# Performance work log

Hardware: AMD Instinct MI355X
Metric: run time of the kernel (lower is better)

Reference implementation:

```python
import jax, jax.numpy as jnp
import numpy as np

B, N, C_IN = 4, 2048, 256
H, C_HEAD = 8, 32  # c_out=256, concat=True -> 256//8=32 per head
ALPHA = 0.2
NEG_INF = -9e15

def glorot(key, shape, fan_in, fan_out):
    lim = jnp.sqrt(6.0 / (fan_in + fan_out))
    return jax.random.uniform(key, shape, jnp.float32, -lim, lim)

def setup_inputs() -> dict:
    key = jax.random.key(0)
    k1, k2, k3, k4, k5 = jax.random.split(key, 5)
    x = jax.random.normal(k1, (B, N, C_IN), jnp.float32)
    G = jax.random.randint(k2, (B, N, N), 0, 2, jnp.int32)
    # ensure self-loops so no row is fully masked
    eye = jnp.eye(N, dtype=jnp.int32)[None]
    G = jnp.maximum(G, eye)
    proj_kernel = glorot(k3, (C_IN, H * C_HEAD), C_IN, H * C_HEAD)
    proj_bias = jnp.zeros((H * C_HEAD,), jnp.float32)
    attn_fst = glorot(k4, (H, C_HEAD), H, C_HEAD)
    attn_snd = glorot(k5, (H, C_HEAD), H, C_HEAD)
    return {"x": x, "G": G, "proj_kernel": proj_kernel, "proj_bias": proj_bias,
            "attn_fst": attn_fst, "attn_snd": attn_snd}

def reference(x, G, proj_kernel, proj_bias, attn_fst, attn_snd):
    b, n = x.shape[0], x.shape[1]
    h = (x @ proj_kernel + proj_bias).reshape(b, n, H, C_HEAD)  # [B,N,H,c]
    lf = jnp.einsum('bnhc,hc->bnh', h, attn_fst)  # [B,N,H]
    ls = jnp.einsum('bnhc,hc->bnh', h, attn_snd)  # [B,N,H]
    logit = lf[:, :, None, :] + ls[:, None, :, :]  # [B,N,N,H]
    logit = jax.nn.leaky_relu(logit, negative_slope=ALPHA)
    logit = jnp.where(G[..., None] == 1, logit, NEG_INF)
    attn = jax.nn.softmax(logit, axis=2)
    out = jnp.einsum('bijh,bjhc->bihc', attn, h)  # [B,N,H,c]
    return out.reshape(b, n, H * C_HEAD)  # concat=True
```

## Files before the change

kernel.cpp:

```cpp
#include <hip/hip_runtime.h>

#define BB 4
#define NN 2048
#define CIN 256
#define HH 8
#define COUT 256
#define ALPHAc 0.2f
#define TI 8
#define CJ 64

#define PBM 128
#define PBN 64
#define PKT 16
#define XLD (PBM + 4)
__global__ __launch_bounds__(256) void gat_proj(
    const float* __restrict__ x, const float* __restrict__ W,
    const float* __restrict__ bias, const float* __restrict__ afst,
    const float* __restrict__ asnd, float* __restrict__ hout,
    float* __restrict__ lfout, float* __restrict__ lsout)
{
    __shared__ float xsT[PKT][XLD];
    __shared__ float wls[PKT][PBN];
    const int t = threadIdx.x;
    const int bx = blockIdx.x & 3;
    const int by = blockIdx.x >> 2;
    const int row0 = by * PBM, col0 = bx * PBN;
    const int tx = t & 15, ty = t >> 4;

    float acc[8][4];
#pragma unroll
    for (int i = 0; i < 8; ++i)
#pragma unroll
        for (int j = 0; j < 4; ++j) acc[i][j] = 0.f;

    for (int kt = 0; kt < CIN; kt += PKT) {
#pragma unroll
        for (int s = 0; s < 2; ++s) {
            const int idx = s * 256 + t;
            const int row = idx >> 2, kq = (idx & 3) * 4;
            const float4 v = *(const float4*)(x + (size_t)(row0 + row) * CIN + kt + kq);
            xsT[kq + 0][row] = v.x; xsT[kq + 1][row] = v.y;
            xsT[kq + 2][row] = v.z; xsT[kq + 3][row] = v.w;
        }
        {
            const int k = t >> 4, c4 = (t & 15) * 4;
            *(float4*)&wls[k][c4] = *(const float4*)(W + (size_t)(kt + k) * COUT + col0 + c4);
        }
        __syncthreads();
#pragma unroll
        for (int k = 0; k < PKT; ++k) {
            float xv[8], wv[4];
            *(float4*)&xv[0] = *(const float4*)&xsT[k][ty * 8];
            *(float4*)&xv[4] = *(const float4*)&xsT[k][ty * 8 + 4];
            *(float4*)&wv[0] = *(const float4*)&wls[k][tx * 4];
#pragma unroll
            for (int i = 0; i < 8; ++i)
#pragma unroll
                for (int j = 0; j < 4; ++j)
                    acc[i][j] = fmaf(xv[i], wv[j], acc[i][j]);
        }
        __syncthreads();
    }

    const float4 bv = *(const float4*)(bias + col0 + tx * 4);
    const float4 af = *(const float4*)(afst + col0 + tx * 4);
    const float4 as = *(const float4*)(asnd + col0 + tx * 4);
    const int hd = (col0 + tx * 4) >> 5;
#pragma unroll
    for (int i = 0; i < 8; ++i) {
        float4 o;
        o.x = acc[i][0] + bv.x; o.y = acc[i][1] + bv.y;
        o.z = acc[i][2] + bv.z; o.w = acc[i][3] + bv.w;
        const int row = row0 + ty * 8 + i;
        *(float4*)(hout + (size_t)row * COUT + col0 + tx * 4) = o;
        float pf = o.x * af.x + o.y * af.y + o.z * af.z + o.w * af.w;
        float ps = o.x * as.x + o.y * as.y + o.z * as.z + o.w * as.w;
#pragma unroll
        for (int off = 1; off < 8; off <<= 1) {
            pf += __shfl_xor(pf, off);
            ps += __shfl_xor(ps, off);
        }
        if ((tx & 7) == 0) {
            lfout[(size_t)row * HH + hd] = pf;
            lsout[(size_t)row * HH + hd] = ps;
        }
    }
}

__device__ __forceinline__ int eoff4(int jl, int h, int half) {
    return jl * 64 + ((((h << 1) + half) ^ (jl & 7)) << 2);
}

__global__ __launch_bounds__(256) void gat_attn(
    const int* __restrict__ G, const float* __restrict__ hin,
    const float* __restrict__ lf, const float* __restrict__ ls,
    float* __restrict__ out)
{
    __shared__ __align__(16) float e_lds[CJ * 64];
    __shared__ unsigned g_lds[4][CJ];
    __shared__ float lf_lds[TI][HH];
    __shared__ float s_lds[TI][HH];

    const int t = threadIdx.x;
    const int b = blockIdx.x / (NN / TI);
    const int i0 = (blockIdx.x % (NN / TI)) * TI;
    const int h = t >> 5;
    const int jj = t & 31;
    const int w = t >> 6;
    const int l = t & 63;
    const int hh = l >> 3;

    if (t < TI * HH)
        lf_lds[t >> 3][t & 7] = lf[(size_t)(b * NN + i0 + (t >> 3)) * HH + (t & 7)];

    float sp[TI];
    float a[TI][4];
#pragma unroll
    for (int r = 0; r < TI; ++r) {
        sp[r] = 0.f;
#pragma unroll
        for (int c2 = 0; c2 < 4; ++c2) a[r][c2] = 0.f;
    }
    __syncthreads();
    float lfv[TI];
#pragma unroll
    for (int r = 0; r < TI; ++r) lfv[r] = lf_lds[r][h];

    for (int j0 = 0; j0 < NN; j0 += CJ) {
        {
            const int col = t & 63;
            const int* gp = G + (size_t)(b * NN + i0 + 2 * w) * NN + j0 + col;
            g_lds[w][col] = (gp[0] != 0 ? 1u : 0u) | (gp[NN] != 0 ? 2u : 0u);
        }
        __syncthreads();
#pragma unroll
        for (int k = 0; k < CJ / 32; ++k) {
            const int jl = jj + 32 * k;
            const float lsv = ls[(size_t)(b * NN + j0 + jl) * HH + h];
            const unsigned gm = g_lds[0][jl] | (g_lds[1][jl] << 2) |
                                (g_lds[2][jl] << 4) | (g_lds[3][jl] << 6);
            float ev[TI];
#pragma unroll
            for (int r = 0; r < TI; ++r) {
                float xv = lfv[r] + lsv;
                xv = xv > 0.f ? xv : ALPHAc * xv;
                ev[r] = ((gm >> r) & 1u) ? __expf(xv) : 0.f;
                sp[r] += ev[r];
            }
            *(float4*)&e_lds[eoff4(jl, h, 0)] = make_float4(ev[0], ev[1], ev[2], ev[3]);
            *(float4*)&e_lds[eoff4(jl, h, 1)] = make_float4(ev[4], ev[5], ev[6], ev[7]);
        }
        __syncthreads();
        {
            const float* hbase = hin + (size_t)(b * NN + j0) * COUT + (l << 2);
            float4 hnext = *(const float4*)(hbase + (size_t)w * COUT);
#pragma unroll
            for (int it = 0; it < CJ / 4; ++it) {
                const int jl = w + it * 4;
                const float4 hv = hnext;
                if (it + 1 < CJ / 4)
                    hnext = *(const float4*)(hbase + (size_t)(jl + 4) * COUT);
                const float4 lo = *(const float4*)&e_lds[eoff4(jl, hh, 0)];
                const float4 hi = *(const float4*)&e_lds[eoff4(jl, hh, 1)];
                const float ee[8] = {lo.x, lo.y, lo.z, lo.w, hi.x, hi.y, hi.z, hi.w};
                const float hvv[4] = {hv.x, hv.y, hv.z, hv.w};
#pragma unroll
                for (int r = 0; r < TI; ++r)
#pragma unroll
                    for (int c2 = 0; c2 < 4; ++c2)
                        a[r][c2] = fmaf(ee[r], hvv[c2], a[r][c2]);
            }
        }
        __syncthreads();
    }
#pragma unroll
    for (int off = 16; off; off >>= 1) {
#pragma unroll
        for (int r = 0; r < TI; ++r) sp[r] += __shfl_xor(sp[r], off);
    }
    if (jj == 0) {
#pragma unroll
        for (int r = 0; r < TI; ++r) s_lds[r][h] = sp[r];
    }
    float* buf = e_lds;
    if (w >= 2) {
#pragma unroll
        for (int r = 0; r < TI; ++r)
#pragma unroll
            for (int c2 = 0; c2 < 4; ++c2)
                buf[((w - 2) << 11) + ((r * 4 + c2) << 6) + l] = a[r][c2];
    }
    __syncthreads();
    if (w < 2) {
#pragma unroll
        for (int r = 0; r < TI; ++r)
#pragma unroll
            for (int c2 = 0; c2 < 4; ++c2)
                a[r][c2] += buf[(w << 11) + ((r * 4 + c2) << 6) + l];
    }
    __syncthreads();
    if (w == 1) {
#pragma unroll
        for (int r = 0; r < TI; ++r)
#pragma unroll
            for (int c2 = 0; c2 < 4; ++c2)
                buf[((r * 4 + c2) << 6) + l] = a[r][c2];
    }
    __syncthreads();
    if (w == 0) {
#pragma unroll
        for (int r = 0; r < TI; ++r) {
            const float inv = 1.f / s_lds[r][hh];
            float4 o;
            o.x = (a[r][0] + buf[((r * 4 + 0) << 6) + l]) * inv;
            o.y = (a[r][1] + buf[((r * 4 + 1) << 6) + l]) * inv;
            o.z = (a[r][2] + buf[((r * 4 + 2) << 6) + l]) * inv;
            o.w = (a[r][3] + buf[((r * 4 + 3) << 6) + l]) * inv;
            *(float4*)(out + (size_t)(b * NN + i0 + r) * COUT + (l << 2)) = o;
        }
    }
}

extern "C" void kernel_launch(void* const* d_in, const int* in_sizes, int n_in,
                              void* d_out, int out_size, void* d_ws, size_t ws_size,
                              hipStream_t stream) {
    const float* x    = (const float*)d_in[0];
    const int*   G    = (const int*)d_in[1];
    const float* W    = (const float*)d_in[2];
    const float* bias = (const float*)d_in[3];
    const float* afst = (const float*)d_in[4];
    const float* asnd = (const float*)d_in[5];
    float* out = (float*)d_out;

    float* h_ws  = (float*)d_ws;
    float* lf_ws = h_ws + (size_t)BB * NN * COUT;
    float* ls_ws = lf_ws + (size_t)BB * NN * HH;

    hipLaunchKernelGGL(gat_proj, dim3((BB * NN / PBM) * (COUT / PBN)), dim3(256),
                       0, stream, x, W, bias, afst, asnd, h_ws, lf_ws, ls_ws);
    hipLaunchKernelGGL(gat_attn, dim3(BB * (NN / TI)), dim3(256), 0, stream,
                       G, h_ws, lf_ws, ls_ws, out);
}
```

Before: 326.8 us.

## Split attention over two j-halves with combine kernel, transpose logits, retile projection

The attention kernel now splits the neighbor dimension into two halves per row block, doubling the grid. Each half writes partial numerators and denominators, and a new combine kernel sums and normalizes them. lf/ls are stored head-major and pre-scaled by log2(e) so that exp2f can be used. The projection GEMM is retiled to smaller 64x32 tiles with a larger k-step, so each thread computes fewer outputs. This adds a third launch and extra partial-buffer traffic in return for more parallelism.

```diff
diff --git a/kernel.cpp b/kernel.cpp
--- a/kernel.cpp
+++ b/kernel.cpp
@@ -5,84 +5,88 @@
 #define CIN 256
 #define HH 8
 #define COUT 256
-#define ALPHAc 0.2f
+#define LOG2E 1.44269504088896340736f
+
+#define PBM 64
+#define PBN 32
+#define PKT 32
 #define TI 8
 #define CJ 64
-
-#define PBM 128
-#define PBN 64
-#define PKT 16
-#define XLD (PBM + 4)
+#define JS 2
+#define JLEN (NN / JS)
+
 __global__ __launch_bounds__(256) void gat_proj(
     const float* __restrict__ x, const float* __restrict__ W,
     const float* __restrict__ bias, const float* __restrict__ afst,
     const float* __restrict__ asnd, float* __restrict__ hout,
-    float* __restrict__ lfout, float* __restrict__ lsout)
+    float* __restrict__ lfT, float* __restrict__ lsT)
 {
-    __shared__ float xsT[PKT][XLD];
-    __shared__ float wls[PKT][PBN];
+    __shared__ float xsT[PKT][PBM + 4];
+    __shared__ float wls[PKT][PBN + 4];
     const int t = threadIdx.x;
-    const int bx = blockIdx.x & 3;
-    const int by = blockIdx.x >> 2;
+    const int bx = blockIdx.x & 7;
+    const int by = blockIdx.x >> 3;
     const int row0 = by * PBM, col0 = bx * PBN;
-    const int tx = t & 15, ty = t >> 4;
-
-    float acc[8][4];
-#pragma unroll
-    for (int i = 0; i < 8; ++i)
-#pragma unroll
-        for (int j = 0; j < 4; ++j) acc[i][j] = 0.f;
+    const int cg = t & 15, rg = t >> 4;
+
+    float acc[4][2];
+#pragma unroll
+    for (int i = 0; i < 4; ++i) { acc[i][0] = 0.f; acc[i][1] = 0.f; }
 
     for (int kt = 0; kt < CIN; kt += PKT) {
 #pragma unroll
         for (int s = 0; s < 2; ++s) {
             const int idx = s * 256 + t;
-            const int row = idx >> 2, kq = (idx & 3) * 4;
+            const int row = idx >> 3, kq = (idx & 7) * 4;
             const float4 v = *(const float4*)(x + (size_t)(row0 + row) * CIN + kt + kq);
             xsT[kq + 0][row] = v.x; xsT[kq + 1][row] = v.y;
             xsT[kq + 2][row] = v.z; xsT[kq + 3][row] = v.w;
         }
         {
-            const int k = t >> 4, c4 = (t & 15) * 4;
+            const int k = t >> 3, c4 = (t & 7) * 4;
             *(float4*)&wls[k][c4] = *(const float4*)(W + (size_t)(kt + k) * COUT + col0 + c4);
         }
         __syncthreads();
 #pragma unroll
         for (int k = 0; k < PKT; ++k) {
-            float xv[8], wv[4];
-            *(float4*)&xv[0] = *(const float4*)&xsT[k][ty * 8];
-            *(float4*)&xv[4] = *(const float4*)&xsT[k][ty * 8 + 4];
-            *(float4*)&wv[0] = *(const float4*)&wls[k][tx * 4];
-#pragma unroll
-            for (int i = 0; i < 8; ++i)
-#pragma unroll
-                for (int j = 0; j < 4; ++j)
-                    acc[i][j] = fmaf(xv[i], wv[j], acc[i][j]);
-        }
-        __syncthreads();
-    }
-
-    const float4 bv = *(const float4*)(bias + col0 + tx * 4);
-    const float4 af = *(const float4*)(afst + col0 + tx * 4);
-    const float4 as = *(const float4*)(asnd + col0 + tx * 4);
-    const int hd = (col0 + tx * 4) >> 5;
-#pragma unroll
-    for (int i = 0; i < 8; ++i) {
-        float4 o;
-        o.x = acc[i][0] + bv.x; o.y = acc[i][1] + bv.y;
-        o.z = acc[i][2] + bv.z; o.w = acc[i][3] + bv.w;
-        const int row = row0 + ty * 8 + i;
-        *(float4*)(hout + (size_t)row * COUT + col0 + tx * 4) = o;
-        float pf = o.x * af.x + o.y * af.y + o.z * af.z + o.w * af.w;
-        float ps = o.x * as.x + o.y * as.y + o.z * as.z + o.w * as.w;
-#pragma unroll
-        for (int off = 1; off < 8; off <<= 1) {
-            pf += __shfl_xor(pf, off);
-            ps += __shfl_xor(ps, off);
-        }
-        if ((tx & 7) == 0) {
-            lfout[(size_t)row * HH + hd] = pf;
-            lsout[(size_t)row * HH + hd] = ps;
+            const float4 xv = *(const float4*)&xsT[k][rg * 4];
+            const float2 wv = *(const float2*)&wls[k][cg * 2];
+#pragma unroll
+            for (int i = 0; i < 4; ++i) {
+                acc[i][0] = fmaf(((const float*)&xv)[i], wv.x, acc[i][0]);
+                acc[i][1] = fmaf(((const float*)&xv)[i], wv.y, acc[i][1]);
+            }
+        }
+        __syncthreads();
+    }
+
+    const float2 bv = *(const float2*)(bias + col0 + cg * 2);
+    const float2 af = *(const float2*)(afst + col0 + cg * 2);
+    const float2 as2 = *(const float2*)(asnd + col0 + cg * 2);
+    const int b = row0 >> 11;
+    float pf[4], ps[4];
+#pragma unroll
+    for (int i = 0; i < 4; ++i) {
+        const float o0 = acc[i][0] + bv.x, o1 = acc[i][1] + bv.y;
+        const int row = row0 + rg * 4 + i;
+        *(float2*)(hout + (size_t)row * COUT + col0 + cg * 2) = make_float2(o0, o1);
+        pf[i] = o0 * af.x + o1 * af.y;
+        ps[i] = o0 * as2.x + o1 * as2.y;
+    }
+#pragma unroll
+    for (int off = 1; off < 16; off <<= 1) {
+#pragma unroll
+        for (int i = 0; i < 4; ++i) {
+            pf[i] += __shfl_xor(pf[i], off);
+            ps[i] += __shfl_xor(ps[i], off);
+        }
+    }
+    if (cg == 0) {
+#pragma unroll
+        for (int i = 0; i < 4; ++i) {
+            const int n = (row0 + rg * 4 + i) & (NN - 1);
+            lfT[(size_t)(b * HH + bx) * NN + n] = pf[i] * LOG2E;
+            lsT[(size_t)(b * HH + bx) * NN + n] = ps[i] * LOG2E;
         }
     }
 }
@@ -93,58 +97,56 @@
 
 __global__ __launch_bounds__(256) void gat_attn(
     const int* __restrict__ G, const float* __restrict__ hin,
-    const float* __restrict__ lf, const float* __restrict__ ls,
-    float* __restrict__ out)
+    const float* __restrict__ lfT, const float* __restrict__ lsT,
+    float* __restrict__ pacc0, float* __restrict__ pacc1,
+    float* __restrict__ pden)
 {
     __shared__ __align__(16) float e_lds[CJ * 64];
     __shared__ unsigned g_lds[4][CJ];
-    __shared__ float lf_lds[TI][HH];
     __shared__ float s_lds[TI][HH];
 
     const int t = threadIdx.x;
-    const int b = blockIdx.x / (NN / TI);
-    const int i0 = (blockIdx.x % (NN / TI)) * TI;
-    const int h = t >> 5;
-    const int jj = t & 31;
-    const int w = t >> 6;
-    const int l = t & 63;
+    const int bi = blockIdx.x >> 1;
+    const int jhalf = blockIdx.x & 1;
+    const int b = bi >> 8;
+    const int i0 = (bi & 255) * TI;
+    const int h = t >> 5, jj = t & 31;
+    const int w = t >> 6, l = t & 63;
     const int hh = l >> 3;
 
-    if (t < TI * HH)
-        lf_lds[t >> 3][t & 7] = lf[(size_t)(b * NN + i0 + (t >> 3)) * HH + (t & 7)];
-
-    float sp[TI];
-    float a[TI][4];
+    float lfv[TI];
+#pragma unroll
+    for (int r = 0; r < TI; ++r)
+        lfv[r] = lfT[(size_t)(b * HH + h) * NN + i0 + r];
+
+    float sp[TI], a[TI][4];
 #pragma unroll
     for (int r = 0; r < TI; ++r) {
         sp[r] = 0.f;
 #pragma unroll
         for (int c2 = 0; c2 < 4; ++c2) a[r][c2] = 0.f;
     }
-    __syncthreads();
-    float lfv[TI];
-#pragma unroll
-    for (int r = 0; r < TI; ++r) lfv[r] = lf_lds[r][h];
-
-    for (int j0 = 0; j0 < NN; j0 += CJ) {
+
+    const int jbeg = jhalf * JLEN;
+    for (int j0 = jbeg; j0 < jbeg + JLEN; j0 += CJ) {
         {
             const int col = t & 63;
-            const int* gp = G + (size_t)(b * NN + i0 + 2 * w) * NN + j0 + col;
+            const int* gp = G + ((size_t)b * NN + i0 + 2 * w) * NN + j0 + col;
             g_lds[w][col] = (gp[0] != 0 ? 1u : 0u) | (gp[NN] != 0 ? 2u : 0u);
         }
         __syncthreads();
 #pragma unroll
         for (int k = 0; k < CJ / 32; ++k) {
             const int jl = jj + 32 * k;
-            const float lsv = ls[(size_t)(b * NN + j0 + jl) * HH + h];
+            const float lsv = lsT[(size_t)(b * HH + h) * NN + j0 + jl];
             const unsigned gm = g_lds[0][jl] | (g_lds[1][jl] << 2) |
                                 (g_lds[2][jl] << 4) | (g_lds[3][jl] << 6);
             float ev[TI];
 #pragma unroll
             for (int r = 0; r < TI; ++r) {
-                float xv = lfv[r] + lsv;
-                xv = xv > 0.f ? xv : ALPHAc * xv;
-                ev[r] = ((gm >> r) & 1u) ? __expf(xv) : 0.f;
+                float s = lfv[r] + lsv;
+                s = fmaxf(s, 0.2f * s);
+                ev[r] = ((gm >> r) & 1u) ? exp2f(s) : 0.f;
                 sp[r] += ev[r];
             }
             *(float4*)&e_lds[eoff4(jl, h, 0)] = make_float4(ev[0], ev[1], ev[2], ev[3]);
@@ -152,7 +154,7 @@
         }
         __syncthreads();
         {
-            const float* hbase = hin + (size_t)(b * NN + j0) * COUT + (l << 2);
+            const float* hbase = hin + ((size_t)b * NN + j0) * COUT + (l << 2);
             float4 hnext = *(const float4*)(hbase + (size_t)w * COUT);
 #pragma unroll
             for (int it = 0; it < CJ / 4; ++it) {
@@ -191,6 +193,9 @@
                 buf[((w - 2) << 11) + ((r * 4 + c2) << 6) + l] = a[r][c2];
     }
     __syncthreads();
+    if (t < TI * HH)
+        pden[((size_t)(b * NN + i0 + (t >> 3)) * JS + jhalf) * HH + (t & 7)] =
+            s_lds[t >> 3][t & 7];
     if (w < 2) {
 #pragma unroll
         for (int r = 0; r < TI; ++r)
@@ -208,17 +213,36 @@
     }
     __syncthreads();
     if (w == 0) {
+        float* pa = jhalf ? pacc1 : pacc0;
 #pragma unroll
         for (int r = 0; r < TI; ++r) {
-            const float inv = 1.f / s_lds[r][hh];
             float4 o;
-            o.x = (a[r][0] + buf[((r * 4 + 0) << 6) + l]) * inv;
-            o.y = (a[r][1] + buf[((r * 4 + 1) << 6) + l]) * inv;
-            o.z = (a[r][2] + buf[((r * 4 + 2) << 6) + l]) * inv;
-            o.w = (a[r][3] + buf[((r * 4 + 3) << 6) + l]) * inv;
-            *(float4*)(out + (size_t)(b * NN + i0 + r) * COUT + (l << 2)) = o;
-        }
-    }
+            o.x = a[r][0] + buf[((r * 4 + 0) << 6) + l];
+            o.y = a[r][1] + buf[((r * 4 + 1) << 6) + l];
+            o.z = a[r][2] + buf[((r * 4 + 2) << 6) + l];
+            o.w = a[r][3] + buf[((r * 4 + 3) << 6) + l];
+            *(float4*)(pa + (size_t)(b * NN + i0 + r) * COUT + (l << 2)) = o;
+        }
+    }
+}
+
+__global__ __launch_bounds__(256) void gat_combine(
+    const float* __restrict__ pacc1, const float* __restrict__ pden,
+    float* __restrict__ out)
+{
+    const int idx = blockIdx.x * 256 + threadIdx.x;
+    const int bi = idx >> 6;
+    const int c4 = (idx & 63) * 4;
+    const int h = c4 >> 5;
+    const float d = pden[(size_t)bi * JS * HH + h] +
+                    pden[((size_t)bi * JS + 1) * HH + h];
+    const float inv = 1.f / d;
+    const float4 p0 = *(const float4*)(out + (size_t)idx * 4);
+    const float4 p1 = *(const float4*)(pacc1 + (size_t)idx * 4);
+    float4 o;
+    o.x = (p0.x + p1.x) * inv; o.y = (p0.y + p1.y) * inv;
+    o.z = (p0.z + p1.z) * inv; o.w = (p0.w + p1.w) * inv;
+    *(float4*)(out + (size_t)idx * 4) = o;
 }
 
 extern "C" void kernel_launch(void* const* d_in, const int* in_sizes, int n_in,
@@ -232,12 +256,16 @@
     const float* asnd = (const float*)d_in[5];
     float* out = (float*)d_out;
 
-    float* h_ws  = (float*)d_ws;
-    float* lf_ws = h_ws + (size_t)BB * NN * COUT;
-    float* ls_ws = lf_ws + (size_t)BB * NN * HH;
+    float* h_ws   = (float*)d_ws;
+    float* lfT_ws = h_ws + (size_t)BB * NN * COUT;
+    float* lsT_ws = lfT_ws + (size_t)BB * HH * NN;
+    float* pacc1  = lsT_ws + (size_t)BB * HH * NN;
+    float* pden   = pacc1 + (size_t)BB * NN * COUT;
 
     hipLaunchKernelGGL(gat_proj, dim3((BB * NN / PBM) * (COUT / PBN)), dim3(256),
-                       0, stream, x, W, bias, afst, asnd, h_ws, lf_ws, ls_ws);
-    hipLaunchKernelGGL(gat_attn, dim3(BB * (NN / TI)), dim3(256), 0, stream,
-                       G, h_ws, lf_ws, ls_ws, out);
-}
+                       0, stream, x, W, bias, afst, asnd, h_ws, lfT_ws, lsT_ws);
+    hipLaunchKernelGGL(gat_attn, dim3(BB * (NN / TI) * JS), dim3(256), 0, stream,
+                       G, h_ws, lfT_ws, lsT_ws, out, pacc1, pden);
+    hipLaunchKernelGGL(gat_combine, dim3(BB * NN * COUT / 4 / 256), dim3(256),
+                       0, stream, pacc1, pden, out);
+}
```

Measured after the change: 374.9 us. 14.7% more time.

## Double-buffer projection GEMM, prefetch mask/logits, transpose lf/ls, fold log2e into logits

Applied to the files above, without the earlier changes.

The projection kernel now double-buffers its x and W tiles in shared memory, issuing global loads for the next k-tile before the current compute. The attention kernel prefetches the next chunk's G mask and ls values into registers during the current chunk and keeps four h rows in flight instead of one. lf/ls are stored head-major so their reads are contiguous, and are prescaled by log2(e) so the kernel can use exp2f and fmaxf for leaky-relu. The cost is more registers and shared memory, which may lower occupancy.

```diff
diff --git a/kernel.cpp b/kernel.cpp
--- a/kernel.cpp
+++ b/kernel.cpp
@@ -5,54 +5,66 @@
 #define CIN 256
 #define HH 8
 #define COUT 256
-#define ALPHAc 0.2f
-#define TI 8
-#define CJ 64
+#define LOG2E 1.44269504088896340736f
 
 #define PBM 128
 #define PBN 64
 #define PKT 16
-#define XLD (PBM + 4)
+#define NKT (CIN / PKT)
+#define TI 8
+#define CJ 64
+#define NC (NN / CJ)
+
 __global__ __launch_bounds__(256) void gat_proj(
     const float* __restrict__ x, const float* __restrict__ W,
     const float* __restrict__ bias, const float* __restrict__ afst,
     const float* __restrict__ asnd, float* __restrict__ hout,
-    float* __restrict__ lfout, float* __restrict__ lsout)
+    float* __restrict__ lfT, float* __restrict__ lsT)
 {
-    __shared__ float xsT[PKT][XLD];
-    __shared__ float wls[PKT][PBN];
+    __shared__ float xsT[2][PKT][PBM + 4];
+    __shared__ float wls[2][PKT][PBN + 4];
     const int t = threadIdx.x;
     const int bx = blockIdx.x & 3;
     const int by = blockIdx.x >> 2;
     const int row0 = by * PBM, col0 = bx * PBN;
     const int tx = t & 15, ty = t >> 4;
 
+    const int srow = t >> 2;
+    const int skq  = (t & 3) * 4;
+    const float* xb0 = x + (size_t)(row0 + srow) * CIN + skq;
+    const float* xb1 = x + (size_t)(row0 + 64 + srow) * CIN + skq;
+    const int swk = t >> 4, swc = (t & 15) * 4;
+    const float* wb = W + (size_t)swk * COUT + col0 + swc;
+
+    float4 xr0 = *(const float4*)xb0;
+    float4 xr1 = *(const float4*)xb1;
+    float4 wr  = *(const float4*)wb;
+    xsT[0][skq+0][srow] = xr0.x; xsT[0][skq+1][srow] = xr0.y;
+    xsT[0][skq+2][srow] = xr0.z; xsT[0][skq+3][srow] = xr0.w;
+    xsT[0][skq+0][64+srow] = xr1.x; xsT[0][skq+1][64+srow] = xr1.y;
+    xsT[0][skq+2][64+srow] = xr1.z; xsT[0][skq+3][64+srow] = xr1.w;
+    *(float4*)&wls[0][swk][swc] = wr;
+    __syncthreads();
+
     float acc[8][4];
 #pragma unroll
     for (int i = 0; i < 8; ++i)
 #pragma unroll
         for (int j = 0; j < 4; ++j) acc[i][j] = 0.f;
 
-    for (int kt = 0; kt < CIN; kt += PKT) {
-#pragma unroll
-        for (int s = 0; s < 2; ++s) {
-            const int idx = s * 256 + t;
-            const int row = idx >> 2, kq = (idx & 3) * 4;
-            const float4 v = *(const float4*)(x + (size_t)(row0 + row) * CIN + kt + kq);
-            xsT[kq + 0][row] = v.x; xsT[kq + 1][row] = v.y;
-            xsT[kq + 2][row] = v.z; xsT[kq + 3][row] = v.w;
-        }
-        {
-            const int k = t >> 4, c4 = (t & 15) * 4;
-            *(float4*)&wls[k][c4] = *(const float4*)(W + (size_t)(kt + k) * COUT + col0 + c4);
-        }
-        __syncthreads();
+    for (int kt = 0; kt < NKT; ++kt) {
+        if (kt + 1 < NKT) {
+            xr0 = *(const float4*)(xb0 + (kt + 1) * PKT);
+            xr1 = *(const float4*)(xb1 + (kt + 1) * PKT);
+            wr  = *(const float4*)(wb + (size_t)(kt + 1) * PKT * COUT);
+        }
+        const int cur = kt & 1;
 #pragma unroll
         for (int k = 0; k < PKT; ++k) {
             float xv[8], wv[4];
-            *(float4*)&xv[0] = *(const float4*)&xsT[k][ty * 8];
-            *(float4*)&xv[4] = *(const float4*)&xsT[k][ty * 8 + 4];
-            *(float4*)&wv[0] = *(const float4*)&wls[k][tx * 4];
+            *(float4*)&xv[0] = *(const float4*)&xsT[cur][k][ty * 8];
+            *(float4*)&xv[4] = *(const float4*)&xsT[cur][k][ty * 8 + 4];
+            *(float4*)&wv[0] = *(const float4*)&wls[cur][k][tx * 4];
 #pragma unroll
             for (int i = 0; i < 8; ++i)
 #pragma unroll
@@ -60,6 +72,15 @@
                     acc[i][j] = fmaf(xv[i], wv[j], acc[i][j]);
         }
         __syncthreads();
+        if (kt + 1 < NKT) {
+            const int nxt = cur ^ 1;
+            xsT[nxt][skq+0][srow] = xr0.x; xsT[nxt][skq+1][srow] = xr0.y;
+            xsT[nxt][skq+2][srow] = xr0.z; xsT[nxt][skq+3][srow] = xr0.w;
+            xsT[nxt][skq+0][64+srow] = xr1.x; xsT[nxt][skq+1][64+srow] = xr1.y;
+            xsT[nxt][skq+2][64+srow] = xr1.z; xsT[nxt][skq+3][64+srow] = xr1.w;
+            *(float4*)&wls[nxt][swk][swc] = wr;
+            __syncthreads();
+        }
     }
 
     const float4 bv = *(const float4*)(bias + col0 + tx * 4);
@@ -81,8 +102,9 @@
             ps += __shfl_xor(ps, off);
         }
         if ((tx & 7) == 0) {
-            lfout[(size_t)row * HH + hd] = pf;
-            lsout[(size_t)row * HH + hd] = ps;
+            const int b = row >> 11, n = row & (NN - 1);
+            lfT[(size_t)(b * HH + hd) * NN + n] = pf * LOG2E;
+            lsT[(size_t)(b * HH + hd) * NN + n] = ps * LOG2E;
         }
     }
 }
@@ -93,73 +115,85 @@
 
 __global__ __launch_bounds__(256) void gat_attn(
     const int* __restrict__ G, const float* __restrict__ hin,
-    const float* __restrict__ lf, const float* __restrict__ ls,
+    const float* __restrict__ lfT, const float* __restrict__ lsT,
     float* __restrict__ out)
 {
     __shared__ __align__(16) float e_lds[CJ * 64];
     __shared__ unsigned g_lds[4][CJ];
-    __shared__ float lf_lds[TI][HH];
     __shared__ float s_lds[TI][HH];
 
     const int t = threadIdx.x;
-    const int b = blockIdx.x / (NN / TI);
-    const int i0 = (blockIdx.x % (NN / TI)) * TI;
-    const int h = t >> 5;
-    const int jj = t & 31;
-    const int w = t >> 6;
-    const int l = t & 63;
+    const int b = blockIdx.x >> 8;
+    const int i0 = (blockIdx.x & 255) * TI;
+    const int h = t >> 5, jj = t & 31;
+    const int w = t >> 6, l = t & 63;
     const int hh = l >> 3;
 
-    if (t < TI * HH)
-        lf_lds[t >> 3][t & 7] = lf[(size_t)(b * NN + i0 + (t >> 3)) * HH + (t & 7)];
-
-    float sp[TI];
-    float a[TI][4];
+    const float* lsrow = lsT + (size_t)(b * HH + h) * NN;
+    float lfv[TI];
+#pragma unroll
+    for (int r = 0; r < TI; ++r)
+        lfv[r] = lfT[(size_t)(b * HH + h) * NN + i0 + r];
+
+    float sp[TI], a[TI][4];
 #pragma unroll
     for (int r = 0; r < TI; ++r) {
         sp[r] = 0.f;
 #pragma unroll
         for (int c2 = 0; c2 < 4; ++c2) a[r][c2] = 0.f;
     }
-    __syncthreads();
-    float lfv[TI];
-#pragma unroll
-    for (int r = 0; r < TI; ++r) lfv[r] = lf_lds[r][h];
-
-    for (int j0 = 0; j0 < NN; j0 += CJ) {
+
+    const int* gbase = G + ((size_t)b * NN + i0 + 2 * w) * NN + l;
+    int g0 = gbase[0], g1 = gbase[NN];
+    float ls0 = lsrow[jj], ls1 = lsrow[32 + jj];
+
+    for (int c = 0; c < NC; ++c) {
+        const int j0 = c * CJ;
+        g_lds[w][l] = (g0 ? 1u : 0u) | (g1 ? 2u : 0u);
+        __syncthreads();
         {
-            const int col = t & 63;
-            const int* gp = G + (size_t)(b * NN + i0 + 2 * w) * NN + j0 + col;
-            g_lds[w][col] = (gp[0] != 0 ? 1u : 0u) | (gp[NN] != 0 ? 2u : 0u);
-        }
-        __syncthreads();
-#pragma unroll
-        for (int k = 0; k < CJ / 32; ++k) {
-            const int jl = jj + 32 * k;
-            const float lsv = ls[(size_t)(b * NN + j0 + jl) * HH + h];
-            const unsigned gm = g_lds[0][jl] | (g_lds[1][jl] << 2) |
-                                (g_lds[2][jl] << 4) | (g_lds[3][jl] << 6);
+            const unsigned gmA = g_lds[0][jj] | (g_lds[1][jj] << 2) |
+                                 (g_lds[2][jj] << 4) | (g_lds[3][jj] << 6);
+            const unsigned gmB = g_lds[0][jj+32] | (g_lds[1][jj+32] << 2) |
+                                 (g_lds[2][jj+32] << 4) | (g_lds[3][jj+32] << 6);
             float ev[TI];
 #pragma unroll
             for (int r = 0; r < TI; ++r) {
-                float xv = lfv[r] + lsv;
-                xv = xv > 0.f ? xv : ALPHAc * xv;
-                ev[r] = ((gm >> r) & 1u) ? __expf(xv) : 0.f;
+                float s = lfv[r] + ls0;
+                s = fmaxf(s, 0.2f * s);
+                ev[r] = ((gmA >> r) & 1u) ? exp2f(s) : 0.f;
                 sp[r] += ev[r];
             }
-            *(float4*)&e_lds[eoff4(jl, h, 0)] = make_float4(ev[0], ev[1], ev[2], ev[3]);
-            *(float4*)&e_lds[eoff4(jl, h, 1)] = make_float4(ev[4], ev[5], ev[6], ev[7]);
-        }
-        __syncthreads();
+            *(float4*)&e_lds[eoff4(jj, h, 0)] = make_float4(ev[0], ev[1], ev[2], ev[3]);
+            *(float4*)&e_lds[eoff4(jj, h, 1)] = make_float4(ev[4], ev[5], ev[6], ev[7]);
+#pragma unroll
+            for (int r = 0; r < TI; ++r) {
+                float s = lfv[r] + ls1;
+                s = fmaxf(s, 0.2f * s);
+                ev[r] = ((gmB >> r) & 1u) ? exp2f(s) : 0.f;
+                sp[r] += ev[r];
+            }
+            *(float4*)&e_lds[eoff4(jj+32, h, 0)] = make_float4(ev[0], ev[1], ev[2], ev[3]);
+            *(float4*)&e_lds[eoff4(jj+32, h, 1)] = make_float4(ev[4], ev[5], ev[6], ev[7]);
+        }
+        __syncthreads();
+        if (c + 1 < NC) {
+            const int* gp = gbase + (size_t)(j0 + CJ);
+            g0 = gp[0]; g1 = gp[NN];
+            ls0 = lsrow[j0 + CJ + jj]; ls1 = lsrow[j0 + CJ + 32 + jj];
+        }
         {
-            const float* hbase = hin + (size_t)(b * NN + j0) * COUT + (l << 2);
-            float4 hnext = *(const float4*)(hbase + (size_t)w * COUT);
+            const float* hbase = hin + ((size_t)b * NN + j0) * COUT + (l << 2);
+            float4 hq[4];
+#pragma unroll
+            for (int p = 0; p < 4; ++p)
+                hq[p] = *(const float4*)(hbase + (size_t)(w + p * 4) * COUT);
 #pragma unroll
             for (int it = 0; it < CJ / 4; ++it) {
                 const int jl = w + it * 4;
-                const float4 hv = hnext;
-                if (it + 1 < CJ / 4)
-                    hnext = *(const float4*)(hbase + (size_t)(jl + 4) * COUT);
+                const float4 hv = hq[it & 3];
+                if (it + 4 < CJ / 4)
+                    hq[it & 3] = *(const float4*)(hbase + (size_t)(jl + 16) * COUT);
                 const float4 lo = *(const float4*)&e_lds[eoff4(jl, hh, 0)];
                 const float4 hi = *(const float4*)&e_lds[eoff4(jl, hh, 1)];
                 const float ee[8] = {lo.x, lo.y, lo.z, lo.w, hi.x, hi.y, hi.z, hi.w};
@@ -232,12 +266,12 @@
     const float* asnd = (const float*)d_in[5];
     float* out = (float*)d_out;
 
-    float* h_ws  = (float*)d_ws;
-    float* lf_ws = h_ws + (size_t)BB * NN * COUT;
-    float* ls_ws = lf_ws + (size_t)BB * NN * HH;
+    float* h_ws   = (float*)d_ws;
+    float* lfT_ws = h_ws + (size_t)BB * NN * COUT;
+    float* lsT_ws = lfT_ws + (size_t)BB * HH * NN;
 
     hipLaunchKernelGGL(gat_proj, dim3((BB * NN / PBM) * (COUT / PBN)), dim3(256),
-                       0, stream, x, W, bias, afst, asnd, h_ws, lf_ws, ls_ws);
+                       0, stream, x, W, bias, afst, asnd, h_ws, lfT_ws, lsT_ws);
     hipLaunchKernelGGL(gat_attn, dim3(BB * (NN / TI)), dim3(256), 0, stream,
-                       G, h_ws, lf_ws, ls_ws, out);
-}
+                       G, h_ws, lfT_ws, lsT_ws, out);
+}
```

Result: faster. 285.4 us (-12.7%).
